# Optimization experiments

Hardware: AMD Instinct MI355X
Metric: run time of the kernel (lower is better)

## Reference

```python
import math
import jax, jax.numpy as jnp
import numpy as np

POS_DIM = 32


def _fourier_features(pos, dim):
    # pos: [B, M] in [0,1] -> [B, M, dim]
    half = dim // 2
    freqs = jnp.exp(jnp.linspace(0.0, math.log(1000.0), half, dtype=pos.dtype))
    ang = pos[..., None] * freqs                      # [B, M, half]
    out = jnp.concatenate([jnp.sin(ang), jnp.cos(ang)], axis=-1)
    if out.shape[-1] < dim:  # pad if dim is odd (not the case for dim=32)
        pad = jnp.zeros(out.shape[:-1] + (dim - out.shape[-1],), dtype=pos.dtype)
        out = jnp.concatenate([out, pad], axis=-1)
    return out


def setup_inputs() -> dict:
    key = jax.random.key(0)
    k1, k2, k3 = jax.random.split(key, 3)
    B, T, D, M = 8, 8192, 512, 512
    frame_emb = jax.random.normal(k1, (B, T, D), dtype=jnp.float32)
    beat_bounds = jax.random.randint(k2, (B, M, 2), 0, T).astype(jnp.int64)
    # nn.Linear(D + POS_DIM, D): store as [in, out] for x @ W + b
    bound = 1.0 / math.sqrt(D + POS_DIM)
    W = jax.random.uniform(k3, (D + POS_DIM, D), dtype=jnp.float32,
                           minval=-bound, maxval=bound)
    b = jnp.zeros((D,), dtype=jnp.float32)
    return {"frame_emb": frame_emb, "beat_bounds": beat_bounds, "W": W, "b": b}


def reference(frame_emb, beat_bounds, W, b):
    B, T, D = frame_emb.shape
    M = beat_bounds.shape[1]
    dt = frame_emb.dtype

    # clamp bounds exactly as the torch loop does
    s = jnp.clip(beat_bounds[..., 0], 0, T - 1)                 # [B, M]
    e = jnp.maximum(s + 1, jnp.minimum(beat_bounds[..., 1], T))  # [B, M]

    # segment mean via exclusive cumsum: sum(frame_emb[b, s:e]) = cs[e] - cs[s]
    cs = jnp.concatenate(
        [jnp.zeros((B, 1, D), dtype=dt), jnp.cumsum(frame_emb, axis=1)], axis=1
    )  # [B, T+1, D]
    seg_sum = (jnp.take_along_axis(cs, e[..., None], axis=1)
               - jnp.take_along_axis(cs, s[..., None], axis=1))   # [B, M, D]
    counts = (e - s).astype(dt)[..., None]
    out = seg_sum / counts

    # fourier position features over beat index
    pos = (jnp.arange(M, dtype=dt) / max(1, M - 1)).clip(0.0, 1.0)  # [M]
    ff = _fourier_features(jnp.broadcast_to(pos[None, :], (B, M)), POS_DIM)
    out = jnp.concatenate([out, ff], axis=-1) @ W + b               # [B, M, D]
    return out
```

## Files before the change

### kernel.cpp

```cpp
#include <hip/hip_runtime.h>
#include <math.h>

#define B 8
#define T 8192
#define D 512
#define M 512
#define POS 32
#define KIN (D + POS)
#define CHUNK 16
#define NCHUNK (T / CHUNK)
#define GRP 16
#define NGRP (NCHUNK / GRP)
#define BM (B * M)

__global__ __launch_bounds__(64) void k_scanchunk(const float* __restrict__ fe,
                                                  float* __restrict__ cp,
                                                  float* __restrict__ gsum) {
    int blk = blockIdx.x;
    int b = blk >> 6;
    int g = (blk >> 1) & 31;
    int h = blk & 1;
    int d4 = (h << 8) + (threadIdx.x << 2);

    const float* src = fe + ((size_t)(b * T + g * (GRP * CHUNK)) * D + d4);
    float* cpb = cp + ((size_t)b * NCHUNK + (size_t)g * GRP) * D + d4;

    float4 acc = {0.f, 0.f, 0.f, 0.f};
#pragma unroll 2
    for (int c = 0; c < GRP; ++c) {
#pragma unroll
        for (int r = 0; r < CHUNK; ++r) {
            float4 v = *(const float4*)(src + (size_t)(c * CHUNK + r) * D);
            acc.x += v.x; acc.y += v.y; acc.z += v.z; acc.w += v.w;
        }
        *(float4*)(cpb + (size_t)c * D) = acc;
    }
    *(float4*)(gsum + ((size_t)b * NGRP + g) * D + d4) = acc;
}

__global__ __launch_bounds__(128) void k_scan_coarse(const float* __restrict__ gsum,
                                                     float* __restrict__ gx) {
    int b = blockIdx.x;
    int d4 = threadIdx.x << 2;
    float4 acc = {0.f, 0.f, 0.f, 0.f};
#pragma unroll
    for (int g = 0; g < NGRP; ++g) {
        *(float4*)(gx + ((size_t)b * (NGRP + 1) + g) * D + d4) = acc;
        float4 v = *(const float4*)(gsum + ((size_t)b * NGRP + g) * D + d4);
        acc.x += v.x; acc.y += v.y; acc.z += v.z; acc.w += v.w;
    }
    *(float4*)(gx + ((size_t)b * (NGRP + 1) + NGRP) * D + d4) = acc;
}

__global__ __launch_bounds__(128) void k_buildx(const float* __restrict__ fe,
                                                const int* __restrict__ bounds,
                                                const float* __restrict__ cp,
                                                const float* __restrict__ gx,
                                                float* __restrict__ X) {
    int bm = blockIdx.x;
    int b = bm / M;
    int m = bm % M;
    int b0 = bounds[bm * 2 + 0];
    int b1 = bounds[bm * 2 + 1];
    int s = min(max(b0, 0), T - 1);
    int e = max(min(b1, T), s + 1);
    int cs_ = s >> 4, ce = e >> 4;
    int d4 = threadIdx.x << 2;

    const float* cpb = cp + (size_t)b * NCHUNK * D;
    const float* gxb = gx + (size_t)b * (NGRP + 1) * D;

    float4 acc = *(const float4*)(gxb + (size_t)(ce >> 4) * D + d4);
    if (ce & 15) {
        float4 v = *(const float4*)(cpb + (size_t)(ce - 1) * D + d4);
        acc.x += v.x; acc.y += v.y; acc.z += v.z; acc.w += v.w;
    }
    {
        float4 p = *(const float4*)(gxb + (size_t)(cs_ >> 4) * D + d4);
        acc.x -= p.x; acc.y -= p.y; acc.z -= p.z; acc.w -= p.w;
        if (cs_ & 15) {
            float4 v = *(const float4*)(cpb + (size_t)(cs_ - 1) * D + d4);
            acc.x -= v.x; acc.y -= v.y; acc.z -= v.z; acc.w -= v.w;
        }
    }

    const float* feb = fe + (size_t)b * T * D + d4;
    for (int t = ce * CHUNK; t < e; ++t) {
        float4 v = *(const float4*)(feb + (size_t)t * D);
        acc.x += v.x; acc.y += v.y; acc.z += v.z; acc.w += v.w;
    }
    for (int t = cs_ * CHUNK; t < s; ++t) {
        float4 v = *(const float4*)(feb + (size_t)t * D);
        acc.x -= v.x; acc.y -= v.y; acc.z -= v.z; acc.w -= v.w;
    }
    float inv = 1.0f / (float)(e - s);
    acc.x *= inv; acc.y *= inv; acc.z *= inv; acc.w *= inv;

    float* xr = X + (size_t)bm * KIN;
    *(float4*)(xr + d4) = acc;

    int t = threadIdx.x;
    if (t < POS) {
        int i = t & 15;
        float freq = expf(0.46051701859880914f * (float)i);
        float pos = (float)m * (1.0f / 511.0f);
        float ang = pos * freq;
        xr[D + t] = (t < 16) ? sinf(ang) : cosf(ang);
    }
}

#define TM 64
#define TN 64
#define TKc 16
__global__ __launch_bounds__(256) void k_gemm(const float* __restrict__ X,
                                              const float* __restrict__ W,
                                              const float* __restrict__ bias,
                                              float* __restrict__ out) {
    __shared__ float Xs[TKc][TM + 4];
    __shared__ float Ws[TKc][TN + 4];
    int n0 = blockIdx.x * TN;
    int m0 = blockIdx.y * TM;
    int tid = threadIdx.x;
    int tx = tid & 15, ty = tid >> 4;

    float acc[4][4] = {{0.f}};

    for (int k0 = 0; k0 < KIN; k0 += TKc) {
        {
            int row = tid >> 2;
            int kq = (tid & 3) << 2;
            float4 v = *(const float4*)(X + (size_t)(m0 + row) * KIN + k0 + kq);
            Xs[kq + 0][row] = v.x;
            Xs[kq + 1][row] = v.y;
            Xs[kq + 2][row] = v.z;
            Xs[kq + 3][row] = v.w;
            float4 w = *(const float4*)(W + (size_t)(k0 + ty) * D + n0 + (tx << 2));
            *(float4*)&Ws[ty][tx << 2] = w;
        }
        __syncthreads();
#pragma unroll
        for (int k = 0; k < TKc; ++k) {
            float4 a = *(const float4*)&Xs[k][ty << 2];
            float4 w4 = *(const float4*)&Ws[k][tx << 2];
            acc[0][0] += a.x * w4.x; acc[0][1] += a.x * w4.y; acc[0][2] += a.x * w4.z; acc[0][3] += a.x * w4.w;
            acc[1][0] += a.y * w4.x; acc[1][1] += a.y * w4.y; acc[1][2] += a.y * w4.z; acc[1][3] += a.y * w4.w;
            acc[2][0] += a.z * w4.x; acc[2][1] += a.z * w4.y; acc[2][2] += a.z * w4.z; acc[2][3] += a.z * w4.w;
            acc[3][0] += a.w * w4.x; acc[3][1] += a.w * w4.y; acc[3][2] += a.w * w4.z; acc[3][3] += a.w * w4.w;
        }
        __syncthreads();
    }

    float4 bv = *(const float4*)(bias + n0 + (tx << 2));
#pragma unroll
    for (int i = 0; i < 4; ++i) {
        float4 o;
        o.x = acc[i][0] + bv.x;
        o.y = acc[i][1] + bv.y;
        o.z = acc[i][2] + bv.z;
        o.w = acc[i][3] + bv.w;
        *(float4*)(out + (size_t)(m0 + (ty << 2) + i) * D + n0 + (tx << 2)) = o;
    }
}

extern "C" void kernel_launch(void* const* d_in, const int* in_sizes, int n_in,
                              void* d_out, int out_size, void* d_ws, size_t ws_size,
                              hipStream_t stream) {
    const float* fe = (const float*)d_in[0];
    const int* bounds = (const int*)d_in[1];
    const float* W = (const float*)d_in[2];
    const float* bias = (const float*)d_in[3];
    float* out = (float*)d_out;

    float* cp = (float*)d_ws;
    float* gsum = cp + (size_t)B * NCHUNK * D;
    float* gx = gsum + (size_t)B * NGRP * D;
    float* X = gx + (size_t)B * (NGRP + 1) * D;

    k_scanchunk<<<B * NGRP * 2, 64, 0, stream>>>(fe, cp, gsum);
    k_scan_coarse<<<B, 128, 0, stream>>>(gsum, gx);
    k_buildx<<<BM, 128, 0, stream>>>(fe, bounds, cp, gx, X);
    dim3 g(D / TN, BM / TM);
    k_gemm<<<g, 256, 0, stream>>>(X, W, bias, out);
}
```

Measured before the change: 267.9 us.

## Use split-bf16 MFMA GEMM and precompute Fourier-feature projection separately

Replaces the fp32 FMA GEMM with a bf16 MFMA GEMM that splits X and W each into high and low bf16 parts and accumulates three products to approximate fp32 accuracy. W is transposed and split by a new kernel on every call. The Fourier-feature part of the linear layer is computed once per beat index into a bias-like table that the GEMM epilogue adds, so the GEMM K shrinks to 512. This adds two kernels and workspace, and the split-bf16 scheme drops the low×low term, giving a slight precision loss.

```diff
diff --git a/kernel.cpp b/kernel.cpp
--- a/kernel.cpp
+++ b/kernel.cpp
@@ -6,12 +6,24 @@
 #define D 512
 #define M 512
 #define POS 32
-#define KIN (D + POS)
 #define CHUNK 16
 #define NCHUNK (T / CHUNK)
 #define GRP 16
 #define NGRP (NCHUNK / GRP)
 #define BM (B * M)
+#define KD 512
+
+typedef __attribute__((ext_vector_type(8))) short short8;
+typedef __attribute__((ext_vector_type(4))) float floatx4;
+
+static __device__ inline unsigned short f2bf(float f) {
+    unsigned int u = __float_as_uint(f);
+    unsigned int r = (u + 0x7fffu + ((u >> 16) & 1u)) >> 16;
+    return (unsigned short)r;
+}
+static __device__ inline float bf2f(unsigned short h) {
+    return __uint_as_float(((unsigned int)h) << 16);
+}
 
 __global__ __launch_bounds__(64) void k_scanchunk(const float* __restrict__ fe,
                                                   float* __restrict__ cp,
@@ -52,14 +64,68 @@
     *(float4*)(gx + ((size_t)b * (NGRP + 1) + NGRP) * D + d4) = acc;
 }
 
+__global__ __launch_bounds__(256) void k_wsplit(const float* __restrict__ W,
+                                                short* __restrict__ WhT,
+                                                short* __restrict__ WlT) {
+    __shared__ float ws[32][65];
+    int k0 = (blockIdx.x & 15) * 32;
+    int n0 = (blockIdx.x >> 4) * 64;
+    int t = threadIdx.x;
+    {
+        int kk = t >> 3;
+        int nn = (t & 7) << 3;
+        const float* src = W + (size_t)(k0 + kk) * D + n0 + nn;
+        float4 v0 = *(const float4*)src;
+        float4 v1 = *(const float4*)(src + 4);
+        ws[kk][nn + 0] = v0.x; ws[kk][nn + 1] = v0.y; ws[kk][nn + 2] = v0.z; ws[kk][nn + 3] = v0.w;
+        ws[kk][nn + 4] = v1.x; ws[kk][nn + 5] = v1.y; ws[kk][nn + 6] = v1.z; ws[kk][nn + 7] = v1.w;
+    }
+    __syncthreads();
+    int n = t >> 2;
+    int kq = (t & 3) << 3;
+    short8 hv, lv;
+#pragma unroll
+    for (int j = 0; j < 8; ++j) {
+        float w = ws[kq + j][n];
+        unsigned short hb = f2bf(w);
+        hv[j] = (short)hb;
+        lv[j] = (short)f2bf(w - bf2f(hb));
+    }
+    size_t off = (size_t)(n0 + n) * KD + k0 + kq;
+    *(short8*)(WhT + off) = hv;
+    *(short8*)(WlT + off) = lv;
+}
+
+__global__ __launch_bounds__(128) void k_ffout(const float* __restrict__ W,
+                                               const float* __restrict__ bias,
+                                               float* __restrict__ ffout) {
+    int m = blockIdx.x;
+    int n4 = threadIdx.x << 2;
+    float pos = (float)m * (1.0f / 511.0f);
+    float4 acc = *(const float4*)(bias + n4);
+#pragma unroll
+    for (int j = 0; j < 16; ++j) {
+        float freq = expf(0.46051701859880914f * (float)j);
+        float ang = pos * freq;
+        float s = sinf(ang), c = cosf(ang);
+        float4 wsn = *(const float4*)(W + (size_t)(D + j) * D + n4);
+        float4 wcn = *(const float4*)(W + (size_t)(D + 16 + j) * D + n4);
+        acc.x += s * wsn.x + c * wcn.x;
+        acc.y += s * wsn.y + c * wcn.y;
+        acc.z += s * wsn.z + c * wcn.z;
+        acc.w += s * wsn.w + c * wcn.w;
+    }
+    *(float4*)(ffout + (size_t)m * D + n4) = acc;
+}
+
 __global__ __launch_bounds__(128) void k_buildx(const float* __restrict__ fe,
                                                 const int* __restrict__ bounds,
                                                 const float* __restrict__ cp,
                                                 const float* __restrict__ gx,
-                                                float* __restrict__ X) {
+                                                short* __restrict__ Xh,
+                                                short* __restrict__ Xl) {
     int bm = blockIdx.x;
     int b = bm / M;
-    int m = bm % M;
     int b0 = bounds[bm * 2 + 0];
     int b1 = bounds[bm * 2 + 1];
     int s = min(max(b0, 0), T - 1);
@@ -94,71 +160,114 @@
         acc.x -= v.x; acc.y -= v.y; acc.z -= v.z; acc.w -= v.w;
     }
     float inv = 1.0f / (float)(e - s);
-    acc.x *= inv; acc.y *= inv; acc.z *= inv; acc.w *= inv;
-
-    float* xr = X + (size_t)bm * KIN;
-    *(float4*)(xr + d4) = acc;
-
-    int t = threadIdx.x;
-    if (t < POS) {
-        int i = t & 15;
-        float freq = expf(0.46051701859880914f * (float)i);
-        float pos = (float)m * (1.0f / 511.0f);
-        float ang = pos * freq;
-        xr[D + t] = (t < 16) ? sinf(ang) : cosf(ang);
-    }
-}
-
-#define TM 64
-#define TN 64
-#define TKc 16
-__global__ __launch_bounds__(256) void k_gemm(const float* __restrict__ X,
-                                              const float* __restrict__ W,
-                                              const float* __restrict__ bias,
+    float x0 = acc.x * inv, x1 = acc.y * inv, x2 = acc.z * inv, x3 = acc.w * inv;
+
+    unsigned short h0 = f2bf(x0), h1 = f2bf(x1), h2 = f2bf(x2), h3 = f2bf(x3);
+    typedef __attribute__((ext_vector_type(4))) short short4v;
+    short4v hv, lv;
+    hv[0] = (short)h0; hv[1] = (short)h1; hv[2] = (short)h2; hv[3] = (short)h3;
+    lv[0] = (short)f2bf(x0 - bf2f(h0));
+    lv[1] = (short)f2bf(x1 - bf2f(h1));
+    lv[2] = (short)f2bf(x2 - bf2f(h2));
+    lv[3] = (short)f2bf(x3 - bf2f(h3));
+    size_t off = (size_t)bm * KD + d4;
+    *(short4v*)(Xh + off) = hv;
+    *(short4v*)(Xl + off) = lv;
+}
+
+__global__ __launch_bounds__(256) void k_gemm(const short* __restrict__ Xh,
+                                              const short* __restrict__ Xl,
+                                              const short* __restrict__ WhT,
+                                              const short* __restrict__ WlT,
+                                              const float* __restrict__ ffout,
                                               float* __restrict__ out) {
-    __shared__ float Xs[TKc][TM + 4];
-    __shared__ float Ws[TKc][TN + 4];
-    int n0 = blockIdx.x * TN;
-    int m0 = blockIdx.y * TM;
+    __shared__ short Ah[64 * 32], Al[64 * 32], Bh[64 * 32], Bl[64 * 32];
+    int n0 = (blockIdx.x & 7) << 6;
+    int m0 = (blockIdx.x >> 3) << 6;
     int tid = threadIdx.x;
-    int tx = tid & 15, ty = tid >> 4;
-
-    float acc[4][4] = {{0.f}};
-
-    for (int k0 = 0; k0 < KIN; k0 += TKc) {
-        {
-            int row = tid >> 2;
-            int kq = (tid & 3) << 2;
-            float4 v = *(const float4*)(X + (size_t)(m0 + row) * KIN + k0 + kq);
-            Xs[kq + 0][row] = v.x;
-            Xs[kq + 1][row] = v.y;
-            Xs[kq + 2][row] = v.z;
-            Xs[kq + 3][row] = v.w;
-            float4 w = *(const float4*)(W + (size_t)(k0 + ty) * D + n0 + (tx << 2));
-            *(float4*)&Ws[ty][tx << 2] = w;
-        }
+    int w = tid >> 6;
+    int l = tid & 63;
+    int lm = l & 15;
+    int q = l >> 4;
+    int wm = (w & 1) << 5;
+    int wn = (w >> 1) << 5;
+
+    floatx4 acc[2][2];
+#pragma unroll
+    for (int i = 0; i < 2; ++i)
+#pragma unroll
+        for (int j = 0; j < 2; ++j)
+            acc[i][j] = (floatx4){0.f, 0.f, 0.f, 0.f};
+
+    int srow = tid >> 2;
+    int skq = tid & 3;
+    int sslot = skq ^ ((srow >> 1) & 3);
+    int ldsoff = (srow << 5) + (sslot << 3);
+    const short* gXh = Xh + (size_t)(m0 + srow) * KD + (skq << 3);
+    const short* gXl = Xl + (size_t)(m0 + srow) * KD + (skq << 3);
+    const short* gBh = WhT + (size_t)(n0 + srow) * KD + (skq << 3);
+    const short* gBl = WlT + (size_t)(n0 + srow) * KD + (skq << 3);
+
+    int aoff[2], boff[2];
+#pragma unroll
+    for (int mt = 0; mt < 2; ++mt) {
+        int row = wm + (mt << 4) + lm;
+        aoff[mt] = (row << 5) + ((q ^ ((row >> 1) & 3)) << 3);
+    }
+#pragma unroll
+    for (int nt = 0; nt < 2; ++nt) {
+        int row = wn + (nt << 4) + lm;
+        boff[nt] = (row << 5) + ((q ^ ((row >> 1) & 3)) << 3);
+    }
+
+    for (int k0 = 0; k0 < KD; k0 += 32) {
+        short8 vxh = *(const short8*)(gXh + k0);
+        short8 vxl = *(const short8*)(gXl + k0);
+        short8 vbh = *(const short8*)(gBh + k0);
+        short8 vbl = *(const short8*)(gBl + k0);
         __syncthreads();
-#pragma unroll
-        for (int k = 0; k < TKc; ++k) {
-            float4 a = *(const float4*)&Xs[k][ty << 2];
-            float4 w4 = *(const float4*)&Ws[k][tx << 2];
-            acc[0][0] += a.x * w4.x; acc[0][1] += a.x * w4.y; acc[0][2] += a.x * w4.z; acc[0][3] += a.x * w4.w;
-            acc[1][0] += a.y * w4.x; acc[1][1] += a.y * w4.y; acc[1][2] += a.y * w4.z; acc[1][3] += a.y * w4.w;
-            acc[2][0] += a.z * w4.x; acc[2][1] += a.z * w4.y; acc[2][2] += a.z * w4.z; acc[2][3] += a.z * w4.w;
-            acc[3][0] += a.w * w4.x; acc[3][1] += a.w * w4.y; acc[3][2] += a.w * w4.z; acc[3][3] += a.w * w4.w;
-        }
+        *(short8*)(Ah + ldsoff) = vxh;
+        *(short8*)(Al + ldsoff) = vxl;
+        *(short8*)(Bh + ldsoff) = vbh;
+        *(short8*)(Bl + ldsoff) = vbl;
         __syncthreads();
-    }
-
-    float4 bv = *(const float4*)(bias + n0 + (tx << 2));
-#pragma unroll
-    for (int i = 0; i < 4; ++i) {
-        float4 o;
-        o.x = acc[i][0] + bv.x;
-        o.y = acc[i][1] + bv.y;
-        o.z = acc[i][2] + bv.z;
-        o.w = acc[i][3] + bv.w;
-        *(float4*)(out + (size_t)(m0 + (ty << 2) + i) * D + n0 + (tx << 2)) = o;
+
+        short8 ah[2], al[2], bh[2], bl[2];
+#pragma unroll
+        for (int mt = 0; mt < 2; ++mt) {
+            ah[mt] = *(const short8*)(Ah + aoff[mt]);
+            al[mt] = *(const short8*)(Al + aoff[mt]);
+        }
+#pragma unroll
+        for (int nt = 0; nt < 2; ++nt) {
+            bh[nt] = *(const short8*)(Bh + boff[nt]);
+            bl[nt] = *(const short8*)(Bl + boff[nt]);
+        }
+#pragma unroll
+        for (int mt = 0; mt < 2; ++mt)
+#pragma unroll
+            for (int nt = 0; nt < 2; ++nt) {
+                acc[mt][nt] = __builtin_amdgcn_mfma_f32_16x16x32_bf16(
+                    ah[mt], bh[nt], acc[mt][nt], 0, 0, 0);
+                acc[mt][nt] = __builtin_amdgcn_mfma_f32_16x16x32_bf16(
+                    ah[mt], bl[nt], acc[mt][nt], 0, 0, 0);
+                acc[mt][nt] = __builtin_amdgcn_mfma_f32_16x16x32_bf16(
+                    al[mt], bh[nt], acc[mt][nt], 0, 0, 0);
+            }
+    }
+
+#pragma unroll
+    for (int mt = 0; mt < 2; ++mt) {
+#pragma unroll
+        for (int nt = 0; nt < 2; ++nt) {
+            int gcol = n0 + wn + (nt << 4) + lm;
+#pragma unroll
+            for (int r = 0; r < 4; ++r) {
+                int grow = m0 + wm + (mt << 4) + (q << 2) + r;
+                float f = ffout[(size_t)(grow & (M - 1)) * D + gcol];
+                out[(size_t)grow * D + gcol] = acc[mt][nt][r] + f;
+            }
+        }
     }
 }
 
@@ -174,11 +283,16 @@
     float* cp = (float*)d_ws;
     float* gsum = cp + (size_t)B * NCHUNK * D;
     float* gx = gsum + (size_t)B * NGRP * D;
-    float* X = gx + (size_t)B * (NGRP + 1) * D;
+    float* ffout = gx + (size_t)B * (NGRP + 1) * D;
+    short* Xh = (short*)(ffout + (size_t)M * D);
+    short* Xl = Xh + (size_t)BM * KD;
+    short* WhT = Xl + (size_t)BM * KD;
+    short* WlT = WhT + (size_t)KD * D;
 
     k_scanchunk<<<B * NGRP * 2, 64, 0, stream>>>(fe, cp, gsum);
     k_scan_coarse<<<B, 128, 0, stream>>>(gsum, gx);
-    k_buildx<<<BM, 128, 0, stream>>>(fe, bounds, cp, gx, X);
-    dim3 g(D / TN, BM / TM);
-    k_gemm<<<g, 256, 0, stream>>>(X, W, bias, out);
-}
+    k_wsplit<<<128, 256, 0, stream>>>(W, WhT, WlT);
+    k_ffout<<<M, 128, 0, stream>>>(W, bias, ffout);
+    k_buildx<<<BM, 128, 0, stream>>>(fe, bounds, cp, gx, Xh, Xl);
+    k_gemm<<<64 * 8, 256, 0, stream>>>(Xh, Xl, WhT, WlT, ffout, out);
+}
```

Result: faster. 248.1 us (-7.4%).
